# Optimization experiments

Measured on AMD Instinct MI355X. Metric: run time of the kernel, lower is better.

Reference implementation:

```python
import jax, jax.numpy as jnp
import numpy as np

N, D_IN, D_OUT = 100000, 256, 256
R, E, B = 8, 40000, 4
LN_EPS = 1e-5


def setup_inputs() -> dict:
    key = jax.random.key(0)
    ks = jax.random.split(key, 6)
    x = jax.random.normal(ks[0], (N, D_IN), dtype=jnp.float32)
    edge_index = jax.random.randint(ks[1], (R, 2, E), 0, N, dtype=jnp.int64)
    bases = jax.random.normal(ks[2], (B, D_IN, D_OUT), dtype=jnp.float32) * 0.01
    coefficients = jax.random.normal(ks[3], (R, B), dtype=jnp.float32) * 0.01
    bound = 1.0 / np.sqrt(D_IN)
    w_self = jax.random.uniform(ks[4], (D_IN, D_OUT), minval=-bound, maxval=bound, dtype=jnp.float32)
    b_self = jax.random.uniform(ks[5], (D_OUT,), minval=-bound, maxval=bound, dtype=jnp.float32)
    ln_gamma = jnp.ones((D_OUT,), dtype=jnp.float32)
    ln_beta = jnp.zeros((D_OUT,), dtype=jnp.float32)
    return {"x": x, "edge_index": edge_index, "bases": bases,
            "coefficients": coefficients, "w_self": w_self, "b_self": b_self,
            "ln_gamma": ln_gamma, "ln_beta": ln_beta}


def reference(x, edge_index, bases, coefficients, w_self, b_self, ln_gamma, ln_beta):
    n = x.shape[0]
    # self loop
    h = x @ w_self + b_self                                   # (N, D_OUT)
    # basis-composed per-relation weights
    W = jnp.einsum('rb,bio->rio', coefficients, bases)        # (R, D_IN, D_OUT)
    src = edge_index[:, 0]                                    # (R, E)
    dst = edge_index[:, 1]                                    # (R, E)
    msg = jnp.einsum('red,rdo->reo', x[src], W)               # (R, E, D_OUT)
    seg = jax.vmap(lambda d, m: jax.ops.segment_sum(m, d, num_segments=n))(dst, msg)
    deg = jax.vmap(lambda d: jax.ops.segment_sum(jnp.ones(d.shape, x.dtype), d, num_segments=n))(dst)
    deg = jnp.maximum(deg, 1.0)                               # clamp(min=1)
    h = h + (seg / deg[..., None]).sum(axis=0)
    # LayerNorm(SiLU(h)); dropout is identity in eval
    a = jax.nn.silu(h)
    mean = a.mean(axis=-1, keepdims=True)
    var = ((a - mean) ** 2).mean(axis=-1, keepdims=True)
    return (a - mean) * jax.lax.rsqrt(var + LN_EPS) * ln_gamma + ln_beta
```

## Files before the change

kernel.cpp:

```cpp
#include <hip/hip_runtime.h>
#include <hip/hip_bf16.h>

#define N_NODES 100000
#define D 256
#define R_REL 8
#define E_EDGES 40000
#define LN_EPS 1e-5f
#define ETOT (R_REL * E_EDGES)
#define SCAN_CH 1024
#define SCAN_NB ((N_NODES + SCAN_CH - 1) / SCAN_CH)
#define NROWT ((N_NODES + 127) / 128)
#define NWG (NROWT * 10)
#define PREPX_NB (N_NODES * D / 8 / 256)
#define PREPB_NB 80
#define COUNT_NB ((ETOT + 255) / 256)

typedef __attribute__((ext_vector_type(8))) short short8;
typedef __attribute__((ext_vector_type(4))) float f32x4;
typedef __attribute__((ext_vector_type(2))) float f32x2;
typedef unsigned char uchar;

__device__ inline ushort bf16u(float f) {
    __hip_bfloat16 h = __float2bfloat16(f);
    return *reinterpret_cast<ushort*>(&h);
}
__device__ inline float bf2f(ushort u) { return __uint_as_float(((unsigned)u) << 16); }

__global__ __launch_bounds__(256) void k_prep(const float* __restrict__ x,
                                              ushort* __restrict__ xb,
                                              const float* __restrict__ w_self,
                                              const float* __restrict__ bases,
                                              ushort* __restrict__ BT,
                                              const int* __restrict__ ei,
                                              int* __restrict__ cntR) {
    __shared__ float tile[64][65];
    int b = blockIdx.x;
    int t = threadIdx.x;
    if (b < PREPX_NB) {
        size_t idx = (size_t)b * 256 + t;
        const float4* xp = (const float4*)(x + idx * 8);
        float4 f0 = xp[0], f1 = xp[1];
        short8 v;
        v[0] = (short)bf16u(f0.x); v[1] = (short)bf16u(f0.y);
        v[2] = (short)bf16u(f0.z); v[3] = (short)bf16u(f0.w);
        v[4] = (short)bf16u(f1.x); v[5] = (short)bf16u(f1.y);
        v[6] = (short)bf16u(f1.z); v[7] = (short)bf16u(f1.w);
        *(short8*)(xb + idx * 8) = v;
    } else if (b < PREPX_NB + PREPB_NB) {
        int bb = b - PREPX_NB;
        int ot = bb >> 2, dt = bb & 3;
        int o0 = ot * 64, d0 = dt * 64;
        int m = o0 >> 8;
        const float* src = (m == 0) ? w_self : bases + (size_t)(m - 1) * D * D;
        int ol0 = o0 & 255;
        int cl = t & 63, rw = t >> 6;
        for (int i = 0; i < 16; ++i) {
            int dl = i * 4 + rw;
            tile[dl][cl] = src[(size_t)(d0 + dl) * D + ol0 + cl];
        }
        __syncthreads();
        for (int i = 0; i < 16; ++i) {
            int ol = i * 4 + rw;
            BT[(size_t)(o0 + ol) * D + d0 + cl] = bf16u(tile[cl][ol]);
        }
    } else {
        int idx = (b - PREPX_NB - PREPB_NB) * 256 + t;
        if (idx < ETOT) {
            int r = idx / E_EDGES, e = idx % E_EDGES;
            int dst = ei[(r * 2 + 1) * E_EDGES + e];
            atomicAdd(&cntR[(size_t)dst * 8 + r], 1);
        }
    }
}

__global__ __launch_bounds__(256) void k_scanA(const int* __restrict__ cntR,
                                               int* __restrict__ start,
                                               int* __restrict__ sumsA) {
    __shared__ int sc[256];
    int t = threadIdx.x;
    int base = blockIdx.x * SCAN_CH + t * 4;
    int v[4];
#pragma unroll
    for (int i = 0; i < 4; ++i) {
        int node = base + i;
        int s = 0;
        if (node < N_NODES) {
            const int4* c = (const int4*)&cntR[(size_t)node * 8];
            int4 a = c[0], b = c[1];
            s = a.x + a.y + a.z + a.w + b.x + b.y + b.z + b.w;
        }
        v[i] = s;
    }
    int ts = v[0] + v[1] + v[2] + v[3];
    sc[t] = ts;
    __syncthreads();
    for (int off = 1; off < 256; off <<= 1) {
        int val = (t >= off) ? sc[t - off] : 0;
        __syncthreads();
        sc[t] += val;
        __syncthreads();
    }
    int excl = sc[t] - ts;
    if (base + 0 < N_NODES) start[base + 0] = excl;
    if (base + 1 < N_NODES) start[base + 1] = excl + v[0];
    if (base + 2 < N_NODES) start[base + 2] = excl + v[0] + v[1];
    if (base + 3 < N_NODES) start[base + 3] = excl + v[0] + v[1] + v[2];
    if (t == 255) sumsA[blockIdx.x] = sc[255];
}

__global__ __launch_bounds__(256) void k_scanC(int* __restrict__ start,
                                               const int* __restrict__ sumsA,
                                               int* __restrict__ cursor) {
    __shared__ int pre[128];
    int t = threadIdx.x;
    if (t < 128) pre[t] = (t < SCAN_NB) ? sumsA[t] : 0;
    __syncthreads();
    for (int off = 1; off < 128; off <<= 1) {
        int val = 0;
        if (t < 128 && t >= off) val = pre[t - off];
        __syncthreads();
        if (t < 128) pre[t] += val;
        __syncthreads();
    }
    int idx = blockIdx.x * blockDim.x + t;
    if (idx < N_NODES) {
        int chunk = idx / SCAN_CH;
        int add = (chunk == 0) ? 0 : pre[chunk - 1];
        int v = start[idx] + add;
        start[idx] = v;
        cursor[idx] = v;
    }
    if (idx == 0) start[N_NODES] = ETOT;
}

__global__ void k_scatter(const int* __restrict__ ei, int* __restrict__ cursor,
                          const int* __restrict__ cntR, int2* __restrict__ pairs) {
    int idx = blockIdx.x * blockDim.x + threadIdx.x;
    if (idx >= ETOT) return;
    int r = idx / E_EDGES, e = idx % E_EDGES;
    int src = ei[r * 2 * E_EDGES + e];
    int dst = ei[(r * 2 + 1) * E_EDGES + e];
    int pos = atomicAdd(&cursor[dst], 1);
    float invd = __builtin_amdgcn_rcpf((float)cntR[(size_t)dst * 8 + r]) * 0.015625f;
    pairs[pos] = make_int2((r << 20) | src, __float_as_int(invd));
}

__global__ __launch_bounds__(256, 2) void k_gemm(const ushort* __restrict__ xb,
                                                 const ushort* __restrict__ BT,
                                                 ushort* __restrict__ hb,
                                                 uchar* __restrict__ U) {
    __shared__ ushort As[2][128 * 64];
    __shared__ ushort Bs[2][128 * 64];
    int t = threadIdx.x;

    const int q = NWG / 8, r8 = NWG % 8;
    int dd = blockIdx.x;
    int xcd = dd & 7, slot = dd >> 3;
    int wgid = (xcd < r8 ? xcd * (q + 1) : r8 * (q + 1) + (xcd - r8) * q) + slot;
    int rowtile = wgid / 10, pass = wgid % 10;
    int row0 = rowtile * 128;

    int l = t & 63, w = t >> 6;
    int wr = w >> 1, wc = w & 1;
    int lr = l & 15, lg = l >> 4;

    auto stageA = [&](int buf, int kt) {
#pragma unroll
        for (int p = 0; p < 4; ++p) {
            int o = p * 4096 + t * 16;
            int rowA = o >> 7;
            int colb = (o & 127) ^ ((rowA & 7) << 4);
            int srcrow = min(row0 + rowA, N_NODES - 1);
            const char* gp = (const char*)xb + ((size_t)srcrow * D + kt * 64) * 2 + colb;
            char* lp = (char*)&As[buf][0] + p * 4096 + (t >> 6) * 1024;
            __builtin_amdgcn_global_load_lds(
                (const __attribute__((address_space(1))) void*)gp,
                (__attribute__((address_space(3))) void*)lp, 16, 0, 0);
        }
    };
    auto stageB = [&](int buf, int kt) {
#pragma unroll
        for (int p = 0; p < 4; ++p) {
            int o = p * 4096 + t * 16;
            int rowB = o >> 7;
            int colb = (o & 127) ^ ((rowB & 7) << 4);
            const char* gp = (const char*)BT +
                ((size_t)(pass * 128 + rowB) * D + kt * 64) * 2 + colb;
            char* lp = (char*)&Bs[buf][0] + p * 4096 + (t >> 6) * 1024;
            __builtin_amdgcn_global_load_lds(
                (const __attribute__((address_space(1))) void*)gp,
                (__attribute__((address_space(3))) void*)lp, 16, 0, 0);
        }
    };

    f32x4 acc[4][4] = {};
    stageA(0, 0); stageB(0, 0);
    stageA(1, 1); stageB(1, 1);
#pragma unroll
    for (int kt = 0; kt < 4; ++kt) {
        int buf = kt & 1;
        if (kt < 3) asm volatile("s_waitcnt vmcnt(8)" ::: "memory");
        else        asm volatile("s_waitcnt vmcnt(0)" ::: "memory");
        __builtin_amdgcn_s_barrier();
        short8 a[2][4], b[2][4];
#pragma unroll
        for (int kk = 0; kk < 2; ++kk) {
            int kb = kk * 64 + lg * 16;
#pragma unroll
            for (int mi = 0; mi < 4; ++mi) {
                int row = wr * 64 + mi * 16 + lr;
                a[kk][mi] = *(const short8*)((const char*)&As[buf][0] +
                             row * 128 + (kb ^ ((row & 7) << 4)));
            }
#pragma unroll
            for (int ni = 0; ni < 4; ++ni) {
                int rb = wc * 64 + ni * 16 + lr;
                b[kk][ni] = *(const short8*)((const char*)&Bs[buf][0] +
                             rb * 128 + (kb ^ ((rb & 7) << 4)));
            }
        }
        asm volatile("s_waitcnt lgkmcnt(0)" ::: "memory");
        __builtin_amdgcn_s_barrier();
        if (kt < 2) { stageA(buf, kt + 2); stageB(buf, kt + 2); }
        __builtin_amdgcn_s_setprio(1);
#pragma unroll
        for (int kk = 0; kk < 2; ++kk)
#pragma unroll
            for (int mi = 0; mi < 4; ++mi)
#pragma unroll
                for (int ni = 0; ni < 4; ++ni)
                    acc[mi][ni] = __builtin_amdgcn_mfma_f32_16x16x32_bf16(
                        a[kk][mi], b[kk][ni], acc[mi][ni], 0, 0, 0);
        __builtin_amdgcn_s_setprio(0);
    }

    if (pass < 2) {
        int qbase = pass * 128 + wc * 64 + lr * 4;
#pragma unroll
        for (int mi = 0; mi < 4; ++mi)
#pragma unroll
            for (int j = 0; j < 4; ++j) {
                int node = row0 + wr * 64 + mi * 16 + lg * 4 + j;
                if (node < N_NODES) {
                    ushort4 v4;
                    v4.x = bf16u(acc[mi][0][j]);
                    v4.y = bf16u(acc[mi][1][j]);
                    v4.z = bf16u(acc[mi][2][j]);
                    v4.w = bf16u(acc[mi][3][j]);
                    *(ushort4*)&hb[(size_t)node * D + qbase] = v4;
                }
            }
    } else {
        int pl = pass - 2;
        int qbase = (pl >> 1) * 256 + (pl & 1) * 128 + wc * 64 + lr * 4;
#pragma unroll
        for (int mi = 0; mi < 4; ++mi)
#pragma unroll
            for (int j = 0; j < 4; ++j) {
                int node = row0 + wr * 64 + mi * 16 + lg * 4 + j;
                if (node < N_NODES) {
                    unsigned d = __builtin_amdgcn_cvt_pk_fp8_f32(
                        acc[mi][0][j] * 64.0f, acc[mi][1][j] * 64.0f, 0, false);
                    d = __builtin_amdgcn_cvt_pk_fp8_f32(
                        acc[mi][2][j] * 64.0f, acc[mi][3][j] * 64.0f, d, true);
                    *(unsigned*)&U[(size_t)node * 1024 + qbase] = d;
                }
            }
    }
}

__global__ __launch_bounds__(256) void k_final(float* __restrict__ out,
                                               const ushort* __restrict__ hb,
                                               const uchar* __restrict__ U,
                                               const int* __restrict__ start,
                                               const int2* __restrict__ pairs,
                                               const float* __restrict__ coeff,
                                               const float* __restrict__ bias,
                                               const float* __restrict__ gamma,
                                               const float* __restrict__ beta) {
    __shared__ float cf[32];
    int t = threadIdx.x;
    if (t < 32) cf[t] = coeff[t];
    __syncthreads();
    int lane = t & 63, w = t >> 6;
    int n = blockIdx.x * 4 + w;
    int s = start[n], e = start[n + 1];

    int c0 = (lane >> 4) * 64 + (lane & 15);
    size_t rowo = (size_t)n * D;
    ushort4 hu = *(const ushort4*)&hb[rowo + lane * 4];
    float bb0 = bias[c0], bb1 = bias[c0 + 16], bb2 = bias[c0 + 32], bb3 = bias[c0 + 48];

    f32x2 a01 = {0.f, 0.f}, a23 = {0.f, 0.f};
    const uchar* Ul = U + lane * 4;

    auto edgemath = [&](int2 c, unsigned v0, unsigned v1, unsigned v2, unsigned v3) {
        float inv = __int_as_float(c.y);
        const float* wv = &cf[(c.x >> 20) * 4];
        f32x2 wp;
        float ww;
        ww = wv[0] * inv; wp[0] = ww; wp[1] = ww;
        a01 += wp * __builtin_amdgcn_cvt_pk_f32_fp8(v0, false);
        a23 += wp * __builtin_amdgcn_cvt_pk_f32_fp8(v0, true);
        ww = wv[1] * inv; wp[0] = ww; wp[1] = ww;
        a01 += wp * __builtin_amdgcn_cvt_pk_f32_fp8(v1, false);
        a23 += wp * __builtin_amdgcn_cvt_pk_f32_fp8(v1, true);
        ww = wv[2] * inv; wp[0] = ww; wp[1] = ww;
        a01 += wp * __builtin_amdgcn_cvt_pk_f32_fp8(v2, false);
        a23 += wp * __builtin_amdgcn_cvt_pk_f32_fp8(v2, true);
        ww = wv[3] * inv; wp[0] = ww; wp[1] = ww;
        a01 += wp * __builtin_amdgcn_cvt_pk_f32_fp8(v3, false);
        a23 += wp * __builtin_amdgcn_cvt_pk_f32_fp8(v3, true);
    };

    int p = s;
    for (; p + 3 < e; p += 4) {
        int2 cA = pairs[p], cB = pairs[p + 1], cC = pairs[p + 2], cD = pairs[p + 3];
        const uchar* uA = Ul + ((size_t)(cA.x & 0xFFFFF) << 10);
        const uchar* uB = Ul + ((size_t)(cB.x & 0xFFFFF) << 10);
        const uchar* uC = Ul + ((size_t)(cC.x & 0xFFFFF) << 10);
        const uchar* uD = Ul + ((size_t)(cD.x & 0xFFFFF) << 10);
        unsigned vA0 = *(const unsigned*)(uA);
        unsigned vA1 = *(const unsigned*)(uA + 256);
        unsigned vA2 = *(const unsigned*)(uA + 512);
        unsigned vA3 = *(const unsigned*)(uA + 768);
        unsigned vB0 = *(const unsigned*)(uB);
        unsigned vB1 = *(const unsigned*)(uB + 256);
        unsigned vB2 = *(const unsigned*)(uB + 512);
        unsigned vB3 = *(const unsigned*)(uB + 768);
        unsigned vC0 = *(const unsigned*)(uC);
        unsigned vC1 = *(const unsigned*)(uC + 256);
        unsigned vC2 = *(const unsigned*)(uC + 512);
        unsigned vC3 = *(const unsigned*)(uC + 768);
        unsigned vD0 = *(const unsigned*)(uD);
        unsigned vD1 = *(const unsigned*)(uD + 256);
        unsigned vD2 = *(const unsigned*)(uD + 512);
        unsigned vD3 = *(const unsigned*)(uD + 768);
        edgemath(cA, vA0, vA1, vA2, vA3);
        edgemath(cB, vB0, vB1, vB2, vB3);
        edgemath(cC, vC0, vC1, vC2, vC3);
        edgemath(cD, vD0, vD1, vD2, vD3);
    }
    for (; p + 1 < e; p += 2) {
        int2 cA = pairs[p], cB = pairs[p + 1];
        const uchar* uA = Ul + ((size_t)(cA.x & 0xFFFFF) << 10);
        const uchar* uB = Ul + ((size_t)(cB.x & 0xFFFFF) << 10);
        unsigned vA0 = *(const unsigned*)(uA);
        unsigned vA1 = *(const unsigned*)(uA + 256);
        unsigned vA2 = *(const unsigned*)(uA + 512);
        unsigned vA3 = *(const unsigned*)(uA + 768);
        unsigned vB0 = *(const unsigned*)(uB);
        unsigned vB1 = *(const unsigned*)(uB + 256);
        unsigned vB2 = *(const unsigned*)(uB + 512);
        unsigned vB3 = *(const unsigned*)(uB + 768);
        edgemath(cA, vA0, vA1, vA2, vA3);
        edgemath(cB, vB0, vB1, vB2, vB3);
    }
    if (p < e) {
        int2 cA = pairs[p];
        const uchar* uA = Ul + ((size_t)(cA.x & 0xFFFFF) << 10);
        unsigned vA0 = *(const unsigned*)(uA);
        unsigned vA1 = *(const unsigned*)(uA + 256);
        unsigned vA2 = *(const unsigned*)(uA + 512);
        unsigned vA3 = *(const unsigned*)(uA + 768);
        edgemath(cA, vA0, vA1, vA2, vA3);
    }

    float a[4];
    a[0] = bf2f(hu.x) + bb0 + a01[0];
    a[1] = bf2f(hu.y) + bb1 + a01[1];
    a[2] = bf2f(hu.z) + bb2 + a23[0];
    a[3] = bf2f(hu.w) + bb3 + a23[1];
    float sum = 0.f, sq = 0.f;
#pragma unroll
    for (int j = 0; j < 4; ++j) {
        float ex = __expf(-a[j]);
        a[j] = a[j] * __builtin_amdgcn_rcpf(1.f + ex);
        sum += a[j]; sq += a[j] * a[j];
    }
#pragma unroll
    for (int off = 32; off >= 1; off >>= 1) {
        sum += __shfl_xor(sum, off, 64);
        sq  += __shfl_xor(sq,  off, 64);
    }
    float mean = sum * (1.0f / 256.0f);
    float var = sq * (1.0f / 256.0f) - mean * mean;
    float rs = rsqrtf(var + LN_EPS);
#pragma unroll
    for (int j = 0; j < 4; ++j) {
        int c = c0 + j * 16;
        out[rowo + c] = (a[j] - mean) * rs * gamma[c] + beta[c];
    }
}

extern "C" void kernel_launch(void* const* d_in, const int* in_sizes, int n_in,
                              void* d_out, int out_size, void* d_ws, size_t ws_size,
                              hipStream_t stream) {
    const float* x      = (const float*)d_in[0];
    const int*   ei     = (const int*)d_in[1];
    const float* bases  = (const float*)d_in[2];
    const float* coeff  = (const float*)d_in[3];
    const float* w_self = (const float*)d_in[4];
    const float* b_self = (const float*)d_in[5];
    const float* gamma  = (const float*)d_in[6];
    const float* beta   = (const float*)d_in[7];
    float* out = (float*)d_out;

    ushort* BT  = (ushort*)d_ws;
    ushort* xb  = BT + (size_t)1280 * D;
    ushort* hb  = xb + (size_t)N_NODES * D;
    uchar*  U   = (uchar*)(hb + (size_t)N_NODES * D);
    int* cntR   = (int*)(U + (size_t)N_NODES * 1024);
    int* start  = cntR + (size_t)R_REL * N_NODES;
    int* cursor = start + N_NODES + 1;
    int* sumsA  = cursor + N_NODES;
    int2* pairs = (int2*)(sumsA + 128);

    hipMemsetAsync(cntR, 0, (size_t)R_REL * N_NODES * sizeof(int), stream);

    k_prep<<<PREPX_NB + PREPB_NB + COUNT_NB, 256, 0, stream>>>(x, xb, w_self,
                                                               bases, BT, ei, cntR);
    k_scanA<<<SCAN_NB, 256, 0, stream>>>(cntR, start, sumsA);
    k_scanC<<<(N_NODES + 255) / 256, 256, 0, stream>>>(start, sumsA, cursor);
    k_scatter<<<(ETOT + 255) / 256, 256, 0, stream>>>(ei, cursor, cntR, pairs);
    k_gemm<<<NWG, 256, 0, stream>>>(xb, BT, hb, U);
    k_final<<<N_NODES / 4, 256, 0, stream>>>(out, hb, U, start, pairs, coeff,
                                             b_self, gamma, beta);
}
```

Before: 231.2 us.

## Fuse fp32-to-bf16 conversion of x into the GEMM A-tile load

Removes the separate pass in k_prep that converted x to a bf16 copy in workspace. The GEMM now loads fp32 x rows into registers one stage ahead, converts them to bf16 and writes them into swizzled LDS. This avoids writing and re-reading the bf16 copy of x. In exchange, each of the 10 output passes per row tile reads twice the bytes for A and repeats the conversion. A-tile staging also becomes a synchronous register-to-LDS write, and the register prefetch buffers add VGPR pressure.

Measured after the change: 265.0 us. 14.6% more time.

```diff
diff --git a/kernel.cpp b/kernel.cpp
--- a/kernel.cpp
+++ b/kernel.cpp
@@ -11,7 +11,6 @@
 #define SCAN_NB ((N_NODES + SCAN_CH - 1) / SCAN_CH)
 #define NROWT ((N_NODES + 127) / 128)
 #define NWG (NROWT * 10)
-#define PREPX_NB (N_NODES * D / 8 / 256)
 #define PREPB_NB 80
 #define COUNT_NB ((ETOT + 255) / 256)
 
@@ -26,9 +25,7 @@
 }
 __device__ inline float bf2f(ushort u) { return __uint_as_float(((unsigned)u) << 16); }
 
-__global__ __launch_bounds__(256) void k_prep(const float* __restrict__ x,
-                                              ushort* __restrict__ xb,
-                                              const float* __restrict__ w_self,
+__global__ __launch_bounds__(256) void k_prep(const float* __restrict__ w_self,
                                               const float* __restrict__ bases,
                                               ushort* __restrict__ BT,
                                               const int* __restrict__ ei,
@@ -36,19 +33,8 @@
     __shared__ float tile[64][65];
     int b = blockIdx.x;
     int t = threadIdx.x;
-    if (b < PREPX_NB) {
-        size_t idx = (size_t)b * 256 + t;
-        const float4* xp = (const float4*)(x + idx * 8);
-        float4 f0 = xp[0], f1 = xp[1];
-        short8 v;
-        v[0] = (short)bf16u(f0.x); v[1] = (short)bf16u(f0.y);
-        v[2] = (short)bf16u(f0.z); v[3] = (short)bf16u(f0.w);
-        v[4] = (short)bf16u(f1.x); v[5] = (short)bf16u(f1.y);
-        v[6] = (short)bf16u(f1.z); v[7] = (short)bf16u(f1.w);
-        *(short8*)(xb + idx * 8) = v;
-    } else if (b < PREPX_NB + PREPB_NB) {
-        int bb = b - PREPX_NB;
-        int ot = bb >> 2, dt = bb & 3;
+    if (b < PREPB_NB) {
+        int ot = b >> 2, dt = b & 3;
         int o0 = ot * 64, d0 = dt * 64;
         int m = o0 >> 8;
         const float* src = (m == 0) ? w_self : bases + (size_t)(m - 1) * D * D;
@@ -64,7 +50,7 @@
             BT[(size_t)(o0 + ol) * D + d0 + cl] = bf16u(tile[cl][ol]);
         }
     } else {
-        int idx = (b - PREPX_NB - PREPB_NB) * 256 + t;
+        int idx = (b - PREPB_NB) * 256 + t;
         if (idx < ETOT) {
             int r = idx / E_EDGES, e = idx % E_EDGES;
             int dst = ei[(r * 2 + 1) * E_EDGES + e];
@@ -145,7 +131,7 @@
     pairs[pos] = make_int2((r << 20) | src, __float_as_int(invd));
 }
 
-__global__ __launch_bounds__(256, 2) void k_gemm(const ushort* __restrict__ xb,
+__global__ __launch_bounds__(256, 2) void k_gemm(const float* __restrict__ x,
                                                  const ushort* __restrict__ BT,
                                                  ushort* __restrict__ hb,
                                                  uchar* __restrict__ U) {
@@ -164,20 +150,6 @@
     int wr = w >> 1, wc = w & 1;
     int lr = l & 15, lg = l >> 4;
 
-    auto stageA = [&](int buf, int kt) {
-#pragma unroll
-        for (int p = 0; p < 4; ++p) {
-            int o = p * 4096 + t * 16;
-            int rowA = o >> 7;
-            int colb = (o & 127) ^ ((rowA & 7) << 4);
-            int srcrow = min(row0 + rowA, N_NODES - 1);
-            const char* gp = (const char*)xb + ((size_t)srcrow * D + kt * 64) * 2 + colb;
-            char* lp = (char*)&As[buf][0] + p * 4096 + (t >> 6) * 1024;
-            __builtin_amdgcn_global_load_lds(
-                (const __attribute__((address_space(1))) void*)gp,
-                (__attribute__((address_space(3))) void*)lp, 16, 0, 0);
-        }
-    };
     auto stageB = [&](int buf, int kt) {
 #pragma unroll
         for (int p = 0; p < 4; ++p) {
@@ -192,15 +164,43 @@
                 (__attribute__((address_space(3))) void*)lp, 16, 0, 0);
         }
     };
+    auto loadA = [&](float4* fa, int kt) {
+#pragma unroll
+        for (int p = 0; p < 4; ++p) {
+            int o = p * 4096 + t * 16;
+            int rowA = o >> 7;
+            int colb = (o & 127) ^ ((rowA & 7) << 4);
+            int srcrow = min(row0 + rowA, N_NODES - 1);
+            const float4* xp = (const float4*)(x + (size_t)srcrow * D + kt * 64 + (colb >> 1));
+            fa[p * 2] = xp[0];
+            fa[p * 2 + 1] = xp[1];
+        }
+    };
+    auto writeA = [&](int buf, const float4* fa) {
+#pragma unroll
+        for (int p = 0; p < 4; ++p) {
+            int o = p * 4096 + t * 16;
+            float4 f0 = fa[p * 2], f1 = fa[p * 2 + 1];
+            short8 v;
+            v[0] = (short)bf16u(f0.x); v[1] = (short)bf16u(f0.y);
+            v[2] = (short)bf16u(f0.z); v[3] = (short)bf16u(f0.w);
+            v[4] = (short)bf16u(f1.x); v[5] = (short)bf16u(f1.y);
+            v[6] = (short)bf16u(f1.z); v[7] = (short)bf16u(f1.w);
+            *(short8*)((char*)&As[buf][0] + o) = v;
+        }
+    };
 
     f32x4 acc[4][4] = {};
-    stageA(0, 0); stageB(0, 0);
-    stageA(1, 1); stageB(1, 1);
+    float4 areg[2][8];
+    stageB(0, 0); loadA(areg[0], 0);
+    stageB(1, 1); loadA(areg[1], 1);
 #pragma unroll
     for (int kt = 0; kt < 4; ++kt) {
         int buf = kt & 1;
-        if (kt < 3) asm volatile("s_waitcnt vmcnt(8)" ::: "memory");
+        if (kt < 3) asm volatile("s_waitcnt vmcnt(12)" ::: "memory");
         else        asm volatile("s_waitcnt vmcnt(0)" ::: "memory");
+        writeA(buf, areg[buf]);
+        asm volatile("s_waitcnt lgkmcnt(0)" ::: "memory");
         __builtin_amdgcn_s_barrier();
         short8 a[2][4], b[2][4];
 #pragma unroll
@@ -221,7 +221,7 @@
         }
         asm volatile("s_waitcnt lgkmcnt(0)" ::: "memory");
         __builtin_amdgcn_s_barrier();
-        if (kt < 2) { stageA(buf, kt + 2); stageB(buf, kt + 2); }
+        if (kt < 2) { stageB(buf, kt + 2); loadA(areg[buf], kt + 2); }
         __builtin_amdgcn_s_setprio(1);
 #pragma unroll
         for (int kk = 0; kk < 2; ++kk)
@@ -407,8 +407,7 @@
     float* out = (float*)d_out;
 
     ushort* BT  = (ushort*)d_ws;
-    ushort* xb  = BT + (size_t)1280 * D;
-    ushort* hb  = xb + (size_t)N_NODES * D;
+    ushort* hb  = BT + (size_t)1280 * D;
     uchar*  U   = (uchar*)(hb + (size_t)N_NODES * D);
     int* cntR   = (int*)(U + (size_t)N_NODES * 1024);
     int* start  = cntR + (size_t)R_REL * N_NODES;
@@ -418,12 +417,11 @@
 
     hipMemsetAsync(cntR, 0, (size_t)R_REL * N_NODES * sizeof(int), stream);
 
-    k_prep<<<PREPX_NB + PREPB_NB + COUNT_NB, 256, 0, stream>>>(x, xb, w_self,
-                                                               bases, BT, ei, cntR);
+    k_prep<<<PREPB_NB + COUNT_NB, 256, 0, stream>>>(w_self, bases, BT, ei, cntR);
     k_scanA<<<SCAN_NB, 256, 0, stream>>>(cntR, start, sumsA);
     k_scanC<<<(N_NODES + 255) / 256, 256, 0, stream>>>(start, sumsA, cursor);
     k_scatter<<<(ETOT + 255) / 256, 256, 0, stream>>>(ei, cursor, cntR, pairs);
-    k_gemm<<<NWG, 256, 0, stream>>>(xb, BT, hb, U);
+    k_gemm<<<NWG, 256, 0, stream>>>(x, BT, hb, U);
     k_final<<<N_NODES / 4, 256, 0, stream>>>(out, hb, U, start, pairs, coeff,
                                              b_self, gamma, beta);
 }
```
